# Kernel optimization log

Measured on AMD Instinct MI355X. Metric: run time of the kernel, lower is better.

Reference implementation:

```python
import jax, jax.numpy as jnp
import numpy as np

HIDDEN = 128
INPUT_SIZE = 64
NUM_ACTIONS = 16
BATCH = 65536


def _uniform(key, shape, scale):
    return jax.random.uniform(key, shape, jnp.float32, -scale, scale)


def setup_inputs() -> dict:
    key = jax.random.key(0)
    ks = jax.random.split(key, 14)
    s = 1.0 / np.sqrt(HIDDEN)  # pytorch LSTM/Linear init scale
    return {
        "x": jax.random.normal(ks[0], (BATCH, INPUT_SIZE), jnp.float32),
        # layer 0 LSTM weights (gate order: i, f, g, o)
        "Wih0": _uniform(ks[1], (4 * HIDDEN, INPUT_SIZE), s),
        "Whh0": _uniform(ks[2], (4 * HIDDEN, HIDDEN), s),
        "bih0": _uniform(ks[3], (4 * HIDDEN,), s),
        "bhh0": _uniform(ks[4], (4 * HIDDEN,), s),
        # layer 1 LSTM weights
        "Wih1": _uniform(ks[5], (4 * HIDDEN, HIDDEN), s),
        "Whh1": _uniform(ks[6], (4 * HIDDEN, HIDDEN), s),
        "bih1": _uniform(ks[7], (4 * HIDDEN,), s),
        "bhh1": _uniform(ks[8], (4 * HIDDEN,), s),
        # policy / value heads
        "Wp": _uniform(ks[9], (NUM_ACTIONS, HIDDEN), s),
        "bp": _uniform(ks[10], (NUM_ACTIONS,), s),
        "Wv": _uniform(ks[11], (1, HIDDEN), s),
        "bv": _uniform(ks[12], (1,), s),
    }


def _lstm_cell(x, h, c, Wih, Whh, bih, bhh):
    # gates: [B, 4H], pytorch gate order i, f, g, o
    g = x @ Wih.T + bih + h @ Whh.T + bhh
    i, f, gg, o = jnp.split(g, 4, axis=-1)
    i = jax.nn.sigmoid(i)
    f = jax.nn.sigmoid(f)
    gg = jnp.tanh(gg)
    o = jax.nn.sigmoid(o)
    c2 = f * c + i * gg
    h2 = o * jnp.tanh(c2)
    return h2, c2


def reference(x, Wih0, Whh0, bih0, bhh0, Wih1, Whh1, bih1, bhh1, Wp, bp, Wv, bv):
    B = x.shape[0]
    z = jnp.zeros((B, HIDDEN), x.dtype)  # state=None -> zero init
    # seq_len == 1: single step through the 2-layer stack
    h0, c0 = _lstm_cell(x, z, z, Wih0, Whh0, bih0, bhh0)
    h1, c1 = _lstm_cell(h0, z, z, Wih1, Whh1, bih1, bhh1)
    out = h1[None]  # [1, B, H] like pytorch LSTM output
    policy = out @ Wp.T + bp  # gumbel=True -> raw logits
    value = out @ Wv.T + bv
    return policy, value
```

## Files before the change

kernel.cpp:

```cpp
#include <hip/hip_runtime.h>
#include <hip/hip_bf16.h>

#define BATCH 65536
#define IN    64
#define H     128
#define NA    16
#define NBLK  256
#define TPB   1024

typedef __bf16 bf16x8 __attribute__((ext_vector_type(8)));
typedef float  f32x4  __attribute__((ext_vector_type(4)));

union Frag { uint4 u; bf16x8 v; };
struct F32x8 { float4 a, b; };

#define EXP2F(v) __builtin_amdgcn_exp2f(v)
#define RCPF(v)  __builtin_amdgcn_rcpf(v)
#define K1 1.442695041f
#define K2 2.885390082f

__device__ __forceinline__ F32x8 ld8f(const float* p) {
    F32x8 r;
    r.a = *reinterpret_cast<const float4*>(p);
    r.b = *reinterpret_cast<const float4*>(p + 4);
    return r;
}
__device__ __forceinline__ Frag cvt8(F32x8 x) {
    Frag f;
    f.v[0]=(__bf16)x.a.x; f.v[1]=(__bf16)x.a.y; f.v[2]=(__bf16)x.a.z; f.v[3]=(__bf16)x.a.w;
    f.v[4]=(__bf16)x.b.x; f.v[5]=(__bf16)x.b.y; f.v[6]=(__bf16)x.b.z; f.v[7]=(__bf16)x.b.w;
    return f;
}
__device__ __forceinline__ Frag cvt44(float4 a, float4 b) {
    Frag f;
    f.v[0]=(__bf16)a.x; f.v[1]=(__bf16)a.y; f.v[2]=(__bf16)a.z; f.v[3]=(__bf16)a.w;
    f.v[4]=(__bf16)b.x; f.v[5]=(__bf16)b.y; f.v[6]=(__bf16)b.z; f.v[7]=(__bf16)b.w;
    return f;
}
__device__ __forceinline__ unsigned pk2(float lo, float hi) {
    unsigned short l = __builtin_bit_cast(unsigned short, (__bf16)lo);
    unsigned short h = __builtin_bit_cast(unsigned short, (__bf16)hi);
    return (unsigned)l | ((unsigned)h << 16);
}
__device__ __forceinline__ float clamp30(float v) {
    return __builtin_fminf(__builtin_fmaxf(v, -30.0f), 30.0f);
}
__device__ __forceinline__ float lstm_h(float ip, float gp, float op) {
    ip = clamp30(ip); gp = clamp30(gp); op = clamp30(op);
    const float Ei = EXP2F(-K1 * ip);
    const float Eg = EXP2F( K2 * gp);
    const float c2 = (Eg - 1.0f) * RCPF((1.0f + Ei) * (Eg + 1.0f));
    const float Eo = EXP2F(-K1 * op);
    const float Ec = EXP2F( K2 * c2);
    return (Ec - 1.0f) * RCPF((1.0f + Eo) * (Ec + 1.0f));
}

__global__ __launch_bounds__(TPB, 4)
void lstm_fused(const float* __restrict__ x,
                const float* __restrict__ Wih0,
                const float* __restrict__ bih0,
                const float* __restrict__ bhh0,
                const float* __restrict__ Wih1,
                const float* __restrict__ bih1,
                const float* __restrict__ bhh1,
                const float* __restrict__ Wp,
                const float* __restrict__ bp,
                const float* __restrict__ Wv,
                const float* __restrict__ bv,
                float* __restrict__ out)
{
    __shared__ __align__(16) uint4 w0s[384 * 8];
    __shared__ __align__(16) uint4 w1s[384 * 16];
    __shared__ __align__(16) uint4 wph[32 * 16];
    __shared__ float b0s[384];
    __shared__ float b1s[384];

    const int tid  = threadIdx.x;
    const int wave = tid >> 6;
    const int lane = tid & 63;
    const int q    = lane >> 4;
    const int m    = lane & 15;
    const int row  = blockIdx.x * 256 + wave * 16 + m;
    const f32x4 vzero = {0.f, 0.f, 0.f, 0.f};

    const float* xp = x + (size_t)row * IN + q * 8;
    F32x8 xr0 = ld8f(xp);
    F32x8 xr1 = ld8f(xp + 32);
    const float4 bpr = *reinterpret_cast<const float4*>(bp + q * 4);
    const float  bvv = bv[0];

#pragma unroll
    for (int r = 0; r < 3; ++r) {
        const int idx = tid + (r << 10);
        const int j = idx >> 3, s = idx & 7;
        const int g = j >> 7, h = j & 127;
        const int srow = h + ((g == 0) ? 0 : (g + 1) * 128);
        Frag f = cvt8(ld8f(Wih0 + (size_t)srow * IN + s * 8));
        w0s[(j << 3) + (s ^ (j & 7))] = f.u;
    }
#pragma unroll
    for (int r = 0; r < 6; ++r) {
        const int idx = tid + (r << 10);
        const int j = idx >> 4, s = idx & 15;
        const int g = j >> 7, h = j & 127;
        const int srow = h + ((g == 0) ? 0 : (g + 1) * 128);
        const int kt = s >> 2, qq = s & 3;
        const float* pA = Wih1 + (size_t)srow * H + kt * 32 + qq * 4;
        Frag f = cvt44(*reinterpret_cast<const float4*>(pA),
                       *reinterpret_cast<const float4*>(pA + 16));
        w1s[(j << 4) + (s ^ (j & 7))] = f.u;
    }
    if (tid < 512) {
        const int j = tid >> 4, s = tid & 15;
        const int kt = s >> 2, qq = s & 3;
        Frag f;
        if (j <= 16) {
            const float* base = (j < 16) ? (Wp + (size_t)j * H) : Wv;
            const float* pA = base + kt * 32 + qq * 4;
            f = cvt44(*reinterpret_cast<const float4*>(pA),
                      *reinterpret_cast<const float4*>(pA + 16));
        } else {
            f.u = make_uint4(0u, 0u, 0u, 0u);
        }
        wph[(j << 4) + (s ^ (j & 7))] = f.u;
    }
    if (tid < 384) {
        const int g = tid >> 7, h = tid & 127;
        const int srow = h + ((g == 0) ? 0 : (g + 1) * 128);
        b0s[tid] = bih0[srow] + bhh0[srow];
    } else if (tid < 768) {
        const int t = tid - 384;
        const int g = t >> 7, h = t & 127;
        const int srow = h + ((g == 0) ? 0 : (g + 1) * 128);
        b1s[t] = bih1[srow] + bhh1[srow];
    }

    __syncthreads();

    const int swz = m & 7;
    Frag xb[2];
    xb[0] = cvt8(xr0);
    xb[1] = cvt8(xr1);

    unsigned hw0[16];
#pragma unroll
    for (int nc = 0; nc < 8; ++nc) {
        f32x4 acc[3]; acc[0] = vzero; acc[1] = vzero; acc[2] = vzero;
#pragma unroll
        for (int g = 0; g < 3; ++g) {
            const int n = g * 128 + nc * 16 + m;
#pragma unroll
            for (int kt = 0; kt < 2; ++kt) {
                Frag a; a.u = w0s[(n << 3) + ((kt * 4 + q) ^ swz)];
                acc[g] = __builtin_amdgcn_mfma_f32_16x16x32_bf16(a.v, xb[kt].v, acc[g], 0, 0, 0);
            }
        }
        const f32x4 bI = *reinterpret_cast<const f32x4*>(b0s +       nc * 16 + q * 4);
        const f32x4 bG = *reinterpret_cast<const f32x4*>(b0s + 128 + nc * 16 + q * 4);
        const f32x4 bO = *reinterpret_cast<const f32x4*>(b0s + 256 + nc * 16 + q * 4);
#pragma unroll
        for (int u = 0; u < 2; ++u) {
            const float ha = lstm_h(acc[0][2*u]   + bI[2*u],   acc[1][2*u]   + bG[2*u],   acc[2][2*u]   + bO[2*u]);
            const float hb = lstm_h(acc[0][2*u+1] + bI[2*u+1], acc[1][2*u+1] + bG[2*u+1], acc[2][2*u+1] + bO[2*u+1]);
            hw0[nc * 2 + u] = pk2(ha, hb);
        }
    }

    unsigned hw1[16];
#pragma unroll
    for (int nc = 0; nc < 8; ++nc) {
        f32x4 acc[3]; acc[0] = vzero; acc[1] = vzero; acc[2] = vzero;
#pragma unroll
        for (int kt = 0; kt < 4; ++kt) {
            Frag b; b.u = make_uint4(hw0[4*kt], hw0[4*kt+1], hw0[4*kt+2], hw0[4*kt+3]);
#pragma unroll
            for (int g = 0; g < 3; ++g) {
                const int n = g * 128 + nc * 16 + m;
                Frag a; a.u = w1s[(n << 4) + ((kt * 4 + q) ^ swz)];
                acc[g] = __builtin_amdgcn_mfma_f32_16x16x32_bf16(a.v, b.v, acc[g], 0, 0, 0);
            }
        }
        const f32x4 bI = *reinterpret_cast<const f32x4*>(b1s +       nc * 16 + q * 4);
        const f32x4 bG = *reinterpret_cast<const f32x4*>(b1s + 128 + nc * 16 + q * 4);
        const f32x4 bO = *reinterpret_cast<const f32x4*>(b1s + 256 + nc * 16 + q * 4);
#pragma unroll
        for (int u = 0; u < 2; ++u) {
            const float ha = lstm_h(acc[0][2*u]   + bI[2*u],   acc[1][2*u]   + bG[2*u],   acc[2][2*u]   + bO[2*u]);
            const float hb = lstm_h(acc[0][2*u+1] + bI[2*u+1], acc[1][2*u+1] + bG[2*u+1], acc[2][2*u+1] + bO[2*u+1]);
            hw1[nc * 2 + u] = pk2(ha, hb);
        }
    }

    f32x4 ap = vzero, av = vzero;
#pragma unroll
    for (int kt = 0; kt < 4; ++kt) {
        Frag b; b.u = make_uint4(hw1[4*kt], hw1[4*kt+1], hw1[4*kt+2], hw1[4*kt+3]);
        Frag a0; a0.u = wph[( m       << 4) + ((kt * 4 + q) ^ swz)];
        ap = __builtin_amdgcn_mfma_f32_16x16x32_bf16(a0.v, b.v, ap, 0, 0, 0);
        Frag a1; a1.u = wph[((16 + m) << 4) + ((kt * 4 + q) ^ swz)];
        av = __builtin_amdgcn_mfma_f32_16x16x32_bf16(a1.v, b.v, av, 0, 0, 0);
    }
    f32x4 po;
    po[0] = ap[0] + bpr.x; po[1] = ap[1] + bpr.y;
    po[2] = ap[2] + bpr.z; po[3] = ap[3] + bpr.w;
    *reinterpret_cast<f32x4*>(out + (size_t)row * NA + q * 4) = po;
    if (q == 0) out[(size_t)BATCH * NA + row] = av[0] + bvv;
}

extern "C" void kernel_launch(void* const* d_in, const int* in_sizes, int n_in,
                              void* d_out, int out_size, void* d_ws, size_t ws_size,
                              hipStream_t stream) {
    lstm_fused<<<dim3(NBLK), dim3(TPB), 0, stream>>>(
        (const float*)d_in[0], (const float*)d_in[1],
        (const float*)d_in[3], (const float*)d_in[4],
        (const float*)d_in[5], (const float*)d_in[7],
        (const float*)d_in[8], (const float*)d_in[9],
        (const float*)d_in[10], (const float*)d_in[11],
        (const float*)d_in[12], (float*)d_out);
}
```

Measured before the change: 107.3 us.

## Process two 16-row subtiles per wave to reuse weight LDS fragments

Halves the threads per block from 1024 to 512 and has each wave handle 32 batch rows as two 16-row subtiles. Each weight fragment read from LDS now feeds two MFMAs, which halves LDS read traffic per row. The per-block weight staging into LDS is split across fewer threads, so setup is slower. The doubled accumulators and hidden-state arrays raise register pressure, and each block has fewer waves to hide latency.

```diff
diff --git a/kernel.cpp b/kernel.cpp
--- a/kernel.cpp
+++ b/kernel.cpp
@@ -6,7 +6,7 @@
 #define H     128
 #define NA    16
 #define NBLK  256
-#define TPB   1024
+#define TPB   512
 
 typedef __bf16 bf16x8 __attribute__((ext_vector_type(8)));
 typedef float  f32x4  __attribute__((ext_vector_type(4)));
@@ -55,7 +55,7 @@
     return (Ec - 1.0f) * RCPF((1.0f + Eo) * (Ec + 1.0f));
 }
 
-__global__ __launch_bounds__(TPB, 4)
+__global__ __launch_bounds__(TPB, 2)
 void lstm_fused(const float* __restrict__ x,
                 const float* __restrict__ Wih0,
                 const float* __restrict__ bih0,
@@ -80,18 +80,22 @@
     const int lane = tid & 63;
     const int q    = lane >> 4;
     const int m    = lane & 15;
-    const int row  = blockIdx.x * 256 + wave * 16 + m;
+    const int rbase = blockIdx.x * 256 + wave * 32;
     const f32x4 vzero = {0.f, 0.f, 0.f, 0.f};
 
-    const float* xp = x + (size_t)row * IN + q * 8;
-    F32x8 xr0 = ld8f(xp);
-    F32x8 xr1 = ld8f(xp + 32);
+    F32x8 xr[2][2];
+#pragma unroll
+    for (int s2 = 0; s2 < 2; ++s2) {
+        const float* xp = x + (size_t)(rbase + s2 * 16 + m) * IN + q * 8;
+        xr[s2][0] = ld8f(xp);
+        xr[s2][1] = ld8f(xp + 32);
+    }
     const float4 bpr = *reinterpret_cast<const float4*>(bp + q * 4);
     const float  bvv = bv[0];
 
 #pragma unroll
-    for (int r = 0; r < 3; ++r) {
-        const int idx = tid + (r << 10);
+    for (int r = 0; r < 6; ++r) {
+        const int idx = tid + (r << 9);
         const int j = idx >> 3, s = idx & 7;
         const int g = j >> 7, h = j & 127;
         const int srow = h + ((g == 0) ? 0 : (g + 1) * 128);
@@ -99,8 +103,8 @@
         w0s[(j << 3) + (s ^ (j & 7))] = f.u;
     }
 #pragma unroll
-    for (int r = 0; r < 6; ++r) {
-        const int idx = tid + (r << 10);
+    for (int r = 0; r < 12; ++r) {
+        const int idx = tid + (r << 9);
         const int j = idx >> 4, s = idx & 15;
         const int g = j >> 7, h = j & 127;
         const int srow = h + ((g == 0) ? 0 : (g + 1) * 128);
@@ -110,7 +114,7 @@
                        *reinterpret_cast<const float4*>(pA + 16));
         w1s[(j << 4) + (s ^ (j & 7))] = f.u;
     }
-    if (tid < 512) {
+    {
         const int j = tid >> 4, s = tid & 15;
         const int kt = s >> 2, qq = s & 3;
         Frag f;
@@ -124,87 +128,129 @@
         }
         wph[(j << 4) + (s ^ (j & 7))] = f.u;
     }
-    if (tid < 384) {
-        const int g = tid >> 7, h = tid & 127;
-        const int srow = h + ((g == 0) ? 0 : (g + 1) * 128);
-        b0s[tid] = bih0[srow] + bhh0[srow];
-    } else if (tid < 768) {
-        const int t = tid - 384;
-        const int g = t >> 7, h = t & 127;
-        const int srow = h + ((g == 0) ? 0 : (g + 1) * 128);
-        b1s[t] = bih1[srow] + bhh1[srow];
+#pragma unroll
+    for (int r = 0; r < 2; ++r) {
+        const int t = tid + (r << 9);
+        if (t < 384) {
+            const int g = t >> 7, h = t & 127;
+            const int srow = h + ((g == 0) ? 0 : (g + 1) * 128);
+            b0s[t] = bih0[srow] + bhh0[srow];
+        } else if (t < 768) {
+            const int tt = t - 384;
+            const int g = tt >> 7, h = tt & 127;
+            const int srow = h + ((g == 0) ? 0 : (g + 1) * 128);
+            b1s[tt] = bih1[srow] + bhh1[srow];
+        }
     }
 
     __syncthreads();
 
     const int swz = m & 7;
-    Frag xb[2];
-    xb[0] = cvt8(xr0);
-    xb[1] = cvt8(xr1);
-
-    unsigned hw0[16];
+    Frag xb[2][2];
+#pragma unroll
+    for (int s2 = 0; s2 < 2; ++s2) {
+        xb[s2][0] = cvt8(xr[s2][0]);
+        xb[s2][1] = cvt8(xr[s2][1]);
+    }
+
+    unsigned hw0[2][16];
 #pragma unroll
     for (int nc = 0; nc < 8; ++nc) {
-        f32x4 acc[3]; acc[0] = vzero; acc[1] = vzero; acc[2] = vzero;
+        f32x4 acc[3][2];
+#pragma unroll
+        for (int g = 0; g < 3; ++g) { acc[g][0] = vzero; acc[g][1] = vzero; }
 #pragma unroll
         for (int g = 0; g < 3; ++g) {
             const int n = g * 128 + nc * 16 + m;
 #pragma unroll
             for (int kt = 0; kt < 2; ++kt) {
                 Frag a; a.u = w0s[(n << 3) + ((kt * 4 + q) ^ swz)];
-                acc[g] = __builtin_amdgcn_mfma_f32_16x16x32_bf16(a.v, xb[kt].v, acc[g], 0, 0, 0);
+#pragma unroll
+                for (int s2 = 0; s2 < 2; ++s2)
+                    acc[g][s2] = __builtin_amdgcn_mfma_f32_16x16x32_bf16(
+                        a.v, xb[s2][kt].v, acc[g][s2], 0, 0, 0);
             }
         }
         const f32x4 bI = *reinterpret_cast<const f32x4*>(b0s +       nc * 16 + q * 4);
         const f32x4 bG = *reinterpret_cast<const f32x4*>(b0s + 128 + nc * 16 + q * 4);
         const f32x4 bO = *reinterpret_cast<const f32x4*>(b0s + 256 + nc * 16 + q * 4);
 #pragma unroll
-        for (int u = 0; u < 2; ++u) {
-            const float ha = lstm_h(acc[0][2*u]   + bI[2*u],   acc[1][2*u]   + bG[2*u],   acc[2][2*u]   + bO[2*u]);
-            const float hb = lstm_h(acc[0][2*u+1] + bI[2*u+1], acc[1][2*u+1] + bG[2*u+1], acc[2][2*u+1] + bO[2*u+1]);
-            hw0[nc * 2 + u] = pk2(ha, hb);
-        }
-    }
-
-    unsigned hw1[16];
+        for (int s2 = 0; s2 < 2; ++s2)
+#pragma unroll
+            for (int u = 0; u < 2; ++u) {
+                const float ha = lstm_h(acc[0][s2][2*u]   + bI[2*u],
+                                        acc[1][s2][2*u]   + bG[2*u],
+                                        acc[2][s2][2*u]   + bO[2*u]);
+                const float hb = lstm_h(acc[0][s2][2*u+1] + bI[2*u+1],
+                                        acc[1][s2][2*u+1] + bG[2*u+1],
+                                        acc[2][s2][2*u+1] + bO[2*u+1]);
+                hw0[s2][nc * 2 + u] = pk2(ha, hb);
+            }
+    }
+
+    unsigned hw1[2][16];
 #pragma unroll
     for (int nc = 0; nc < 8; ++nc) {
-        f32x4 acc[3]; acc[0] = vzero; acc[1] = vzero; acc[2] = vzero;
+        f32x4 acc[3][2];
+#pragma unroll
+        for (int g = 0; g < 3; ++g) { acc[g][0] = vzero; acc[g][1] = vzero; }
 #pragma unroll
         for (int kt = 0; kt < 4; ++kt) {
-            Frag b; b.u = make_uint4(hw0[4*kt], hw0[4*kt+1], hw0[4*kt+2], hw0[4*kt+3]);
+            Frag b[2];
+#pragma unroll
+            for (int s2 = 0; s2 < 2; ++s2)
+                b[s2].u = make_uint4(hw0[s2][4*kt], hw0[s2][4*kt+1],
+                                     hw0[s2][4*kt+2], hw0[s2][4*kt+3]);
 #pragma unroll
             for (int g = 0; g < 3; ++g) {
                 const int n = g * 128 + nc * 16 + m;
                 Frag a; a.u = w1s[(n << 4) + ((kt * 4 + q) ^ swz)];
-                acc[g] = __builtin_amdgcn_mfma_f32_16x16x32_bf16(a.v, b.v, acc[g], 0, 0, 0);
+#pragma unroll
+                for (int s2 = 0; s2 < 2; ++s2)
+                    acc[g][s2] = __builtin_amdgcn_mfma_f32_16x16x32_bf16(
+                        a.v, b[s2].v, acc[g][s2], 0, 0, 0);
             }
         }
         const f32x4 bI = *reinterpret_cast<const f32x4*>(b1s +       nc * 16 + q * 4);
         const f32x4 bG = *reinterpret_cast<const f32x4*>(b1s + 128 + nc * 16 + q * 4);
         const f32x4 bO = *reinterpret_cast<const f32x4*>(b1s + 256 + nc * 16 + q * 4);
 #pragma unroll
-        for (int u = 0; u < 2; ++u) {
-            const float ha = lstm_h(acc[0][2*u]   + bI[2*u],   acc[1][2*u]   + bG[2*u],   acc[2][2*u]   + bO[2*u]);
-            const float hb = lstm_h(acc[0][2*u+1] + bI[2*u+1], acc[1][2*u+1] + bG[2*u+1], acc[2][2*u+1] + bO[2*u+1]);
-            hw1[nc * 2 + u] = pk2(ha, hb);
-        }
-    }
-
-    f32x4 ap = vzero, av = vzero;
+        for (int s2 = 0; s2 < 2; ++s2)
+#pragma unroll
+            for (int u = 0; u < 2; ++u) {
+                const float ha = lstm_h(acc[0][s2][2*u]   + bI[2*u],
+                                        acc[1][s2][2*u]   + bG[2*u],
+                                        acc[2][s2][2*u]   + bO[2*u]);
+                const float hb = lstm_h(acc[0][s2][2*u+1] + bI[2*u+1],
+                                        acc[1][s2][2*u+1] + bG[2*u+1],
+                                        acc[2][s2][2*u+1] + bO[2*u+1]);
+                hw1[s2][nc * 2 + u] = pk2(ha, hb);
+            }
+    }
+
+    f32x4 ap[2], av[2];
+    ap[0] = vzero; ap[1] = vzero; av[0] = vzero; av[1] = vzero;
 #pragma unroll
     for (int kt = 0; kt < 4; ++kt) {
-        Frag b; b.u = make_uint4(hw1[4*kt], hw1[4*kt+1], hw1[4*kt+2], hw1[4*kt+3]);
         Frag a0; a0.u = wph[( m       << 4) + ((kt * 4 + q) ^ swz)];
-        ap = __builtin_amdgcn_mfma_f32_16x16x32_bf16(a0.v, b.v, ap, 0, 0, 0);
         Frag a1; a1.u = wph[((16 + m) << 4) + ((kt * 4 + q) ^ swz)];
-        av = __builtin_amdgcn_mfma_f32_16x16x32_bf16(a1.v, b.v, av, 0, 0, 0);
-    }
-    f32x4 po;
-    po[0] = ap[0] + bpr.x; po[1] = ap[1] + bpr.y;
-    po[2] = ap[2] + bpr.z; po[3] = ap[3] + bpr.w;
-    *reinterpret_cast<f32x4*>(out + (size_t)row * NA + q * 4) = po;
-    if (q == 0) out[(size_t)BATCH * NA + row] = av[0] + bvv;
+#pragma unroll
+        for (int s2 = 0; s2 < 2; ++s2) {
+            Frag b; b.u = make_uint4(hw1[s2][4*kt], hw1[s2][4*kt+1],
+                                     hw1[s2][4*kt+2], hw1[s2][4*kt+3]);
+            ap[s2] = __builtin_amdgcn_mfma_f32_16x16x32_bf16(a0.v, b.v, ap[s2], 0, 0, 0);
+            av[s2] = __builtin_amdgcn_mfma_f32_16x16x32_bf16(a1.v, b.v, av[s2], 0, 0, 0);
+        }
+    }
+#pragma unroll
+    for (int s2 = 0; s2 < 2; ++s2) {
+        const int row = rbase + s2 * 16 + m;
+        f32x4 po;
+        po[0] = ap[s2][0] + bpr.x; po[1] = ap[s2][1] + bpr.y;
+        po[2] = ap[s2][2] + bpr.z; po[3] = ap[s2][3] + bpr.w;
+        *reinterpret_cast<f32x4*>(out + (size_t)row * NA + q * 4) = po;
+        if (q == 0) out[(size_t)BATCH * NA + row] = av[s2][0] + bvv;
+    }
 }
 
 extern "C" void kernel_launch(void* const* d_in, const int* in_sizes, int n_in,
```

Result: no change. 107.3 us (-0.0%).
